# Optimization experiments

Measured on AMD Instinct MI355X. Metric: run time of the kernel, lower is better.

## Reference

```python
import jax, jax.numpy as jnp
import numpy as np

B, S, D, BS = 256, 256, 448, 32
NB = D // BS  # 14 diagonal blocks


def setup_inputs() -> dict:
    key = jax.random.key(0)
    ks = jax.random.split(key, 9)
    xavier = float(np.sqrt(6.0 / (D + D)))
    inp = {
        "x": jax.random.normal(ks[0], (B, S, D), jnp.float32),
        "W_q": jax.random.uniform(ks[1], (D, D), jnp.float32, -xavier, xavier),
        "W_k": jax.random.uniform(ks[2], (D, D), jnp.float32, -xavier, xavier),
        "W_v": jax.random.uniform(ks[3], (D, D), jnp.float32, -xavier, xavier),
        "W_o": jax.random.uniform(ks[4], (D, D), jnp.float32, -xavier, xavier),
        "SSM_A": jnp.tril(jax.random.normal(ks[5], (D, D), jnp.float32) * 0.001),
        "SSM_B": jnp.tril(jax.random.normal(ks[6], (D, D), jnp.float32) * 0.001),
        "SSM_C": jnp.tril(jax.random.normal(ks[7], (D, D), jnp.float32) * 0.001),
        "dynamic_weight": jnp.full((1,), 0.5, jnp.float32),  # torch init value
        "ln_gamma": jnp.ones((D,), jnp.float32),
        "ln_beta": jnp.zeros((D,), jnp.float32),
    }
    return inp


def _diag_blocks(M):
    # extract the NB diagonal 32x32 blocks: [NB, BS, BS]
    idx = jnp.arange(NB)
    return M.reshape(NB, BS, NB, BS)[idx, :, idx, :]


def _block_linear(x, M):
    # block-diagonal matmul, vectorized over all 14 blocks at once
    xr = x.reshape(B, S, NB, BS)
    return jnp.einsum('bsni,nij->bsnj', xr, _diag_blocks(M)).reshape(B, S, D)


def _block_quadratic(x, M):
    # einsum('bsi,ij,bsk->bsj') per block == (x_blk @ M_blk) * sum_k(x_blk) * 0.1
    xr = x.reshape(B, S, NB, BS)
    y = jnp.einsum('bsni,nij->bsnj', xr, _diag_blocks(M))
    y = y * (jnp.sum(xr, axis=-1, keepdims=True) * 0.1)
    return y.reshape(B, S, D)


def _layer_norm(x, gamma, beta):
    mu = jnp.mean(x, axis=-1, keepdims=True)
    var = jnp.mean(jnp.square(x - mu), axis=-1, keepdims=True)
    return (x - mu) * jax.lax.rsqrt(var + 1e-5) * gamma + beta


def reference(x, W_q, W_k, W_v, W_o, SSM_A, SSM_B, SSM_C, dynamic_weight, ln_gamma, ln_beta):
    q = jnp.einsum('bsi,id->bsd', x, W_q)
    k = jnp.einsum('bsi,id->bsd', x, W_k)
    v = jnp.einsum('bsi,id->bsd', x, W_v)
    dw = jax.nn.sigmoid(dynamic_weight)  # sigmoid(0.5)=0.622 -> blended branch (seq_len == threshold)
    ssm_lin = _layer_norm(
        _block_linear(q, SSM_A) + _block_linear(k, SSM_B) + _block_linear(v, SSM_C),
        ln_gamma, ln_beta)
    ssm_quad = _layer_norm(
        _block_quadratic(q, SSM_A) + _block_quadratic(k, SSM_B) + _block_quadratic(v, SSM_C),
        ln_gamma, ln_beta)
    ssm = dw * ssm_quad + (1.0 - dw) * ssm_lin
    ssm = ssm + x  # residual; dropout is identity in eval mode
    return jnp.einsum('bsd,do->bso', ssm, W_o)
```

## Files before the change

kernel.cpp:

```cpp
#include <hip/hip_runtime.h>
#include <hip/hip_bf16.h>


typedef unsigned short u16;
typedef unsigned int u32;
typedef __bf16 bf16x8 __attribute__((ext_vector_type(8)));
typedef float f32x4 __attribute__((ext_vector_type(4)));

#define D_DIM 448
#define M_DIM 65536
#define NCAT 1386
#define NCAT_PAD 1408
#define N2_PAD 512

__device__ __forceinline__ u16 f2bf(float f) {
    union { float f; u32 u; } v; v.f = f;
    u32 u = v.u;
    u32 r = (u + 0x7fffu + ((u >> 16) & 1u)) >> 16;
    return (u16)r;
}
__device__ __forceinline__ float bf2f(u16 h) {
    union { u32 u; float f; } v; v.u = ((u32)h) << 16;
    return v.f;
}

__device__ __forceinline__ void load_lds16(const void* g, void* l) {
    __builtin_amdgcn_global_load_lds(
        (const __attribute__((address_space(1))) void*)g,
        (__attribute__((address_space(3))) void*)l, 16, 0, 0);
}

__global__ __launch_bounds__(64) void prep_wcat(
    const float* __restrict__ Wq, const float* __restrict__ Wk, const float* __restrict__ Wv,
    const float* __restrict__ SA, const float* __restrict__ SB, const float* __restrict__ SC,
    u16* __restrict__ WcatT)
{
    const int j = blockIdx.x;
    const int lane = threadIdx.x;
    u16* dst = WcatT + (size_t)j * D_DIM;

    if (j >= NCAT) {
        for (int t = lane; t < D_DIM; t += 64) dst[t] = 0;
        return;
    }
    if (j < 3 * D_DIM) {
        const int g = j / D_DIM, jj = j % D_DIM, n = jj >> 5;
        const float* W = (g == 0) ? Wq : (g == 1) ? Wk : Wv;
        const float* Mm = (g == 0) ? SA : (g == 1) ? SB : SC;
        __shared__ float av[32];
        if (lane < 32) av[lane] = Mm[(size_t)(n * 32 + lane) * D_DIM + jj];
        __syncthreads();
        for (int t = lane; t < D_DIM; t += 64) {
            const float* wrow = W + (size_t)t * D_DIM + n * 32;
            float s = 0.f;
            #pragma unroll
            for (int l = 0; l < 32; ++l) s += wrow[l] * av[l];
            dst[t] = f2bf(s);
        }
    } else {
        const int js = j - 3 * D_DIM;
        const int g = js / 14, n = js % 14;
        const float* W = (g == 0) ? Wq : (g == 1) ? Wk : Wv;
        for (int t = lane; t < D_DIM; t += 64) {
            const float* wrow = W + (size_t)t * D_DIM + n * 32;
            float s = 0.f;
            #pragma unroll
            for (int l = 0; l < 32; ++l) s += wrow[l];
            dst[t] = f2bf(0.1f * s);
        }
    }
}

__global__ __launch_bounds__(256) void prep_wo(const float* __restrict__ Wo, u16* __restrict__ WoT) {
    const int idx = blockIdx.x * 256 + threadIdx.x;
    const int o = idx / D_DIM, d = idx % D_DIM;
    WoT[idx] = (o < D_DIM) ? f2bf(Wo[(size_t)d * D_DIM + o]) : (u16)0;
}

__global__ __launch_bounds__(256) void cvt_x_kernel(const float* __restrict__ x, u16* __restrict__ xb) {
    const size_t i = ((size_t)blockIdx.x * 256 + threadIdx.x) * 4;
    float4 v = *reinterpret_cast<const float4*>(x + i);
    u16 o0 = f2bf(v.x), o1 = f2bf(v.y), o2 = f2bf(v.z), o3 = f2bf(v.w);
    u32 lo = (u32)o0 | ((u32)o1 << 16);
    u32 hi = (u32)o2 | ((u32)o3 << 16);
    u32* p = reinterpret_cast<u32*>(xb + i);
    p[0] = lo; p[1] = hi;
}

template<bool BF16OUT>
__global__ __launch_bounds__(256) void gemm_bt(
    const u16* __restrict__ A,
    const u16* __restrict__ Bt,
    void* __restrict__ Cout,
    int ldc, int nreal, int ncolblk)
{
    __shared__ u16 lA[2][128 * 32];
    __shared__ u16 lB[2][128 * 32];
    const int tid = threadIdx.x;
    const int wave = tid >> 6, lane = tid & 63;

    const int cpx = gridDim.x >> 3;
    const int bid = blockIdx.x;
    const int t = (bid & 7) * cpx + (bid >> 3);
    const int bx = t % ncolblk, by = t / ncolblk;
    const int brow = by * 128, bcol = bx * 128;
    const int wr = wave >> 1, wc = wave & 1;

    f32x4 acc[4][4];
    #pragma unroll
    for (int i = 0; i < 4; ++i)
        #pragma unroll
        for (int j = 0; j < 4; ++j) {
            f32x4 z = {0.f, 0.f, 0.f, 0.f};
            acc[i][j] = z;
        }

    const int lrow = lane & 15;
    const int kgrp = (lane >> 4) << 3;

    for (int kt = 0; kt < 7; ++kt) {
        const int k0 = kt * 64;
        #pragma unroll
        for (int ks = 0; ks < 2; ++ks) {
            const int kb = k0 + ks * 32;
            #pragma unroll
            for (int i = 0; i < 2; ++i) {
                const int chunk = (wave * 2 + i) * 64 + lane;
                const int row = chunk >> 2, kk = (chunk & 3) << 3;
                load_lds16(A + (size_t)(brow + row) * D_DIM + kb + kk,
                           &lA[ks][(wave * 2 + i) * 512]);
                load_lds16(Bt + (size_t)(bcol + row) * D_DIM + kb + kk,
                           &lB[ks][(wave * 2 + i) * 512]);
            }
        }
        __syncthreads();

        #pragma unroll
        for (int ks = 0; ks < 2; ++ks) {
            bf16x8 af[4];
            #pragma unroll
            for (int mi = 0; mi < 4; ++mi) {
                const int r = wr * 64 + mi * 16 + lrow;
                af[mi] = *reinterpret_cast<const bf16x8*>(&lA[ks][r * 32 + kgrp]);
            }
            #pragma unroll
            for (int ni = 0; ni < 4; ++ni) {
                const int n = wc * 64 + ni * 16 + lrow;
                bf16x8 bfr = *reinterpret_cast<const bf16x8*>(&lB[ks][n * 32 + kgrp]);
                #pragma unroll
                for (int mi = 0; mi < 4; ++mi)
                    acc[mi][ni] = __builtin_amdgcn_mfma_f32_16x16x32_bf16(af[mi], bfr, acc[mi][ni], 0, 0, 0);
            }
        }
        __syncthreads();
    }

    const int rbase = brow + wr * 64 + ((lane >> 4) << 2);
    const int cbase = bcol + wc * 64 + (lane & 15);
    #pragma unroll
    for (int mi = 0; mi < 4; ++mi) {
        #pragma unroll
        for (int ni = 0; ni < 4; ++ni) {
            const int col = cbase + ni * 16;
            #pragma unroll
            for (int r = 0; r < 4; ++r) {
                const int row = rbase + mi * 16 + r;
                const float v = acc[mi][ni][r];
                if (BF16OUT) {
                    ((u16*)Cout)[(size_t)row * ldc + col] = f2bf(v);
                } else {
                    if (col < nreal)
                        ((float*)Cout)[(size_t)row * nreal + col] = v;
                }
            }
        }
    }
}

__global__ __launch_bounds__(256) void ssm_epilogue(
    const u16* __restrict__ Z, const u16* __restrict__ xb,
    const float* __restrict__ gamma, const float* __restrict__ beta,
    const float* __restrict__ dynw, u16* __restrict__ ssm)
{
    const int row = blockIdx.x * 4 + (threadIdx.x >> 6);
    const int lane = threadIdx.x & 63;
    const u16* zr = Z + (size_t)row * NCAT_PAD;
    const float dwv = 1.0f / (1.0f + __expf(-dynw[0]));
    const bool act = lane < 56;
    const int j0 = lane * 8;
    const int n = lane >> 2;

    float sv = (lane < 42) ? bf2f(zr[1344 + lane]) : 0.f;
    const float sA = __shfl(sv, n);
    const float sB = __shfl(sv, 14 + n);
    const float sC = __shfl(sv, 28 + n);

    float L[8], Q[8];
    float s0 = 0.f, s1 = 0.f, s2 = 0.f, s3 = 0.f;
    if (act) {
        uint4 va = *reinterpret_cast<const uint4*>(zr + j0);
        uint4 vb = *reinterpret_cast<const uint4*>(zr + 448 + j0);
        uint4 vc = *reinterpret_cast<const uint4*>(zr + 896 + j0);
        const u32* pa = reinterpret_cast<const u32*>(&va);
        const u32* pb = reinterpret_cast<const u32*>(&vb);
        const u32* pc = reinterpret_cast<const u32*>(&vc);
        #pragma unroll
        for (int w = 0; w < 4; ++w) {
            #pragma unroll
            for (int h = 0; h < 2; ++h) {
                const int i = w * 2 + h;
                const float a = bf2f((u16)((pa[w] >> (16 * h)) & 0xffffu));
                const float b = bf2f((u16)((pb[w] >> (16 * h)) & 0xffffu));
                const float c = bf2f((u16)((pc[w] >> (16 * h)) & 0xffffu));
                const float Lv = a + b + c;
                const float Qv = a * sA + b * sB + c * sC;
                L[i] = Lv; Q[i] = Qv;
                s0 += Lv; s1 += Lv * Lv; s2 += Qv; s3 += Qv * Qv;
            }
        }
    } else {
        #pragma unroll
        for (int i = 0; i < 8; ++i) { L[i] = 0.f; Q[i] = 0.f; }
    }
    #pragma unroll
    for (int off = 32; off > 0; off >>= 1) {
        s0 += __shfl_xor(s0, off);
        s1 += __shfl_xor(s1, off);
        s2 += __shfl_xor(s2, off);
        s3 += __shfl_xor(s3, off);
    }
    const float inv = 1.0f / 448.0f;
    const float mu0 = s0 * inv, mu1 = s2 * inv;
    const float rs0 = rsqrtf(fmaxf(s1 * inv - mu0 * mu0, 0.f) + 1e-5f);
    const float rs1 = rsqrtf(fmaxf(s3 * inv - mu1 * mu1, 0.f) + 1e-5f);

    if (act) {
        float4 g0 = *reinterpret_cast<const float4*>(gamma + j0);
        float4 g1 = *reinterpret_cast<const float4*>(gamma + j0 + 4);
        float4 b0 = *reinterpret_cast<const float4*>(beta + j0);
        float4 b1 = *reinterpret_cast<const float4*>(beta + j0 + 4);
        const float* gp = &g0.x;
        float gv[8] = {g0.x, g0.y, g0.z, g0.w, g1.x, g1.y, g1.z, g1.w};
        float bv[8] = {b0.x, b0.y, b0.z, b0.w, b1.x, b1.y, b1.z, b1.w};
        (void)gp;
        uint4 vx = *reinterpret_cast<const uint4*>(xb + (size_t)row * D_DIM + j0);
        const u32* px = reinterpret_cast<const u32*>(&vx);
        u32 outw[4];
        #pragma unroll
        for (int w = 0; w < 4; ++w) {
            u16 h0, h1;
            {
                const int i = w * 2;
                const float xr = bf2f((u16)(px[w] & 0xffffu));
                const float ln = (L[i] - mu0) * rs0 * gv[i] + bv[i];
                const float qn = (Q[i] - mu1) * rs1 * gv[i] + bv[i];
                h0 = f2bf(dwv * qn + (1.0f - dwv) * ln + xr);
            }
            {
                const int i = w * 2 + 1;
                const float xr = bf2f((u16)(px[w] >> 16));
                const float ln = (L[i] - mu0) * rs0 * gv[i] + bv[i];
                const float qn = (Q[i] - mu1) * rs1 * gv[i] + bv[i];
                h1 = f2bf(dwv * qn + (1.0f - dwv) * ln + xr);
            }
            outw[w] = (u32)h0 | ((u32)h1 << 16);
        }
        uint4 ov = {outw[0], outw[1], outw[2], outw[3]};
        *reinterpret_cast<uint4*>(ssm + (size_t)row * D_DIM + j0) = ov;
    }
}

extern "C" void kernel_launch(void* const* d_in, const int* in_sizes, int n_in,
                              void* d_out, int out_size, void* d_ws, size_t ws_size,
                              hipStream_t stream) {
    const float* x    = (const float*)d_in[0];
    const float* Wq   = (const float*)d_in[1];
    const float* Wk   = (const float*)d_in[2];
    const float* Wv   = (const float*)d_in[3];
    const float* Wo   = (const float*)d_in[4];
    const float* SA   = (const float*)d_in[5];
    const float* SB   = (const float*)d_in[6];
    const float* SC   = (const float*)d_in[7];
    const float* dynw = (const float*)d_in[8];
    const float* gma  = (const float*)d_in[9];
    const float* bta  = (const float*)d_in[10];
    float* out = (float*)d_out;

    char* ws = (char*)d_ws;
    u16* Xbf   = (u16*)(ws);
    u16* WcatT = (u16*)(ws + 58720256);
    u16* WoT   = (u16*)(ws + 59981824);
    u16* Z     = (u16*)(ws + 60440576);

    prep_wcat<<<dim3(NCAT_PAD), dim3(64), 0, stream>>>(Wq, Wk, Wv, SA, SB, SC, WcatT);
    prep_wo<<<dim3(896), dim3(256), 0, stream>>>(Wo, WoT);
    cvt_x_kernel<<<dim3(28672), dim3(256), 0, stream>>>(x, Xbf);

    gemm_bt<true><<<dim3(5632), dim3(256), 0, stream>>>(
        Xbf, WcatT, (void*)Z, NCAT_PAD, NCAT_PAD, 11);

    ssm_epilogue<<<dim3(M_DIM / 4), dim3(256), 0, stream>>>(Z, Xbf, gma, bta, dynw, Xbf);

    gemm_bt<false><<<dim3(2048), dim3(256), 0, stream>>>(
        Xbf, WoT, (void*)out, 448, 448, 4);
}
```

Measured before the change: 449.0 us.

## Merge prep kernels into one launch and double-buffer GEMM k-loop

Folds the three preprocessing kernels (x conversion, W_o transpose, Wcat build) into one kernel dispatched by block index, which saves two launches. The GEMM k-loop now uses ping-pong LDS buffers with 32-wide k stages, so global-to-LDS loads for the next stage are issued before the MFMAs on the current stage. This overlaps memory and compute, but the loop runs 14 stages instead of 7, which adds barriers. In the merged prep kernel the Wcat blocks now run 256 threads where only 64 were used before, so many threads sit idle.

```diff
diff --git a/kernel.cpp b/kernel.cpp
--- a/kernel.cpp
+++ b/kernel.cpp
@@ -13,6 +13,10 @@
 #define NCAT_PAD 1408
 #define N2_PAD 512
 
+#define CVT_BLKS 28672
+#define WO_BLKS 896
+#define WCAT_BLKS 1408
+
 __device__ __forceinline__ u16 f2bf(float f) {
     union { float f; u32 u; } v; v.f = f;
     u32 u = v.u;
@@ -30,17 +34,35 @@
         (__attribute__((address_space(3))) void*)l, 16, 0, 0);
 }
 
-__global__ __launch_bounds__(64) void prep_wcat(
+__global__ __launch_bounds__(256) void prep_all(
+    const float* __restrict__ x,
     const float* __restrict__ Wq, const float* __restrict__ Wk, const float* __restrict__ Wv,
+    const float* __restrict__ Wo,
     const float* __restrict__ SA, const float* __restrict__ SB, const float* __restrict__ SC,
-    u16* __restrict__ WcatT)
+    u16* __restrict__ Xbf, u16* __restrict__ WcatT, u16* __restrict__ WoT)
 {
-    const int j = blockIdx.x;
-    const int lane = threadIdx.x;
+    const int bid = blockIdx.x;
+    const int tid = threadIdx.x;
+
+    if (bid < CVT_BLKS) {
+        const size_t i = ((size_t)bid * 256 + tid) * 4;
+        float4 v = *reinterpret_cast<const float4*>(x + i);
+        u32 lo = (u32)f2bf(v.x) | ((u32)f2bf(v.y) << 16);
+        u32 hi = (u32)f2bf(v.z) | ((u32)f2bf(v.w) << 16);
+        u32* p = reinterpret_cast<u32*>(Xbf + i);
+        p[0] = lo; p[1] = hi;
+        return;
+    }
+    if (bid < CVT_BLKS + WO_BLKS) {
+        const int idx = (bid - CVT_BLKS) * 256 + tid;
+        const int o = idx / D_DIM, d = idx % D_DIM;
+        WoT[idx] = (o < D_DIM) ? f2bf(Wo[(size_t)d * D_DIM + o]) : (u16)0;
+        return;
+    }
+    const int j = bid - (CVT_BLKS + WO_BLKS);
     u16* dst = WcatT + (size_t)j * D_DIM;
-
     if (j >= NCAT) {
-        for (int t = lane; t < D_DIM; t += 64) dst[t] = 0;
+        for (int t = tid; t < D_DIM; t += 256) dst[t] = 0;
         return;
     }
     if (j < 3 * D_DIM) {
@@ -48,9 +70,9 @@
         const float* W = (g == 0) ? Wq : (g == 1) ? Wk : Wv;
         const float* Mm = (g == 0) ? SA : (g == 1) ? SB : SC;
         __shared__ float av[32];
-        if (lane < 32) av[lane] = Mm[(size_t)(n * 32 + lane) * D_DIM + jj];
+        if (tid < 32) av[tid] = Mm[(size_t)(n * 32 + tid) * D_DIM + jj];
         __syncthreads();
-        for (int t = lane; t < D_DIM; t += 64) {
+        for (int t = tid; t < D_DIM; t += 256) {
             const float* wrow = W + (size_t)t * D_DIM + n * 32;
             float s = 0.f;
             #pragma unroll
@@ -61,7 +83,7 @@
         const int js = j - 3 * D_DIM;
         const int g = js / 14, n = js % 14;
         const float* W = (g == 0) ? Wq : (g == 1) ? Wk : Wv;
-        for (int t = lane; t < D_DIM; t += 64) {
+        for (int t = tid; t < D_DIM; t += 256) {
             const float* wrow = W + (size_t)t * D_DIM + n * 32;
             float s = 0.f;
             #pragma unroll
@@ -69,22 +91,6 @@
             dst[t] = f2bf(0.1f * s);
         }
     }
-}
-
-__global__ __launch_bounds__(256) void prep_wo(const float* __restrict__ Wo, u16* __restrict__ WoT) {
-    const int idx = blockIdx.x * 256 + threadIdx.x;
-    const int o = idx / D_DIM, d = idx % D_DIM;
-    WoT[idx] = (o < D_DIM) ? f2bf(Wo[(size_t)d * D_DIM + o]) : (u16)0;
-}
-
-__global__ __launch_bounds__(256) void cvt_x_kernel(const float* __restrict__ x, u16* __restrict__ xb) {
-    const size_t i = ((size_t)blockIdx.x * 256 + threadIdx.x) * 4;
-    float4 v = *reinterpret_cast<const float4*>(x + i);
-    u16 o0 = f2bf(v.x), o1 = f2bf(v.y), o2 = f2bf(v.z), o3 = f2bf(v.w);
-    u32 lo = (u32)o0 | ((u32)o1 << 16);
-    u32 hi = (u32)o2 | ((u32)o3 << 16);
-    u32* p = reinterpret_cast<u32*>(xb + i);
-    p[0] = lo; p[1] = hi;
 }
 
 template<bool BF16OUT>
@@ -94,8 +100,7 @@
     void* __restrict__ Cout,
     int ldc, int nreal, int ncolblk)
 {
-    __shared__ u16 lA[2][128 * 32];
-    __shared__ u16 lB[2][128 * 32];
+    __shared__ u16 lA0[4096], lB0[4096], lA1[4096], lB1[4096];
     const int tid = threadIdx.x;
     const int wave = tid >> 6, lane = tid & 63;
 
@@ -110,50 +115,58 @@
     #pragma unroll
     for (int i = 0; i < 4; ++i)
         #pragma unroll
-        for (int j = 0; j < 4; ++j) {
+        for (int jj = 0; jj < 4; ++jj) {
             f32x4 z = {0.f, 0.f, 0.f, 0.f};
-            acc[i][j] = z;
+            acc[i][jj] = z;
         }
 
     const int lrow = lane & 15;
     const int kgrp = (lane >> 4) << 3;
 
-    for (int kt = 0; kt < 7; ++kt) {
-        const int k0 = kt * 64;
-        #pragma unroll
-        for (int ks = 0; ks < 2; ++ks) {
-            const int kb = k0 + ks * 32;
-            #pragma unroll
-            for (int i = 0; i < 2; ++i) {
-                const int chunk = (wave * 2 + i) * 64 + lane;
-                const int row = chunk >> 2, kk = (chunk & 3) << 3;
-                load_lds16(A + (size_t)(brow + row) * D_DIM + kb + kk,
-                           &lA[ks][(wave * 2 + i) * 512]);
-                load_lds16(Bt + (size_t)(bcol + row) * D_DIM + kb + kk,
-                           &lB[ks][(wave * 2 + i) * 512]);
-            }
-        }
+    const int c0 = wave * 128 + lane;
+    const int c1 = c0 + 64;
+    const int row0 = c0 >> 2, kk0 = (c0 & 3) << 3;
+    const int row1 = c1 >> 2, kk1 = (c1 & 3) << 3;
+    const u16* ga0 = A  + (size_t)(brow + row0) * D_DIM + kk0;
+    const u16* ga1 = A  + (size_t)(brow + row1) * D_DIM + kk1;
+    const u16* gb0 = Bt + (size_t)(bcol + row0) * D_DIM + kk0;
+    const u16* gb1 = Bt + (size_t)(bcol + row1) * D_DIM + kk1;
+    const int d0 = wave * 1024, d1 = wave * 1024 + 512;
+
+#define STAGE(LA, LB, koff) do { \
+    load_lds16(ga0 + (koff), &LA[d0]); \
+    load_lds16(ga1 + (koff), &LA[d1]); \
+    load_lds16(gb0 + (koff), &LB[d0]); \
+    load_lds16(gb1 + (koff), &LB[d1]); \
+} while (0)
+
+#define COMPUTE(LA, LB) do { \
+    bf16x8 af[4]; \
+    _Pragma("unroll") \
+    for (int mi = 0; mi < 4; ++mi) \
+        af[mi] = *reinterpret_cast<const bf16x8*>(&LA[(wr * 64 + mi * 16 + lrow) * 32 + kgrp]); \
+    _Pragma("unroll") \
+    for (int ni = 0; ni < 4; ++ni) { \
+        bf16x8 bfr = *reinterpret_cast<const bf16x8*>(&LB[(wc * 64 + ni * 16 + lrow) * 32 + kgrp]); \
+        _Pragma("unroll") \
+        for (int mi = 0; mi < 4; ++mi) \
+            acc[mi][ni] = __builtin_amdgcn_mfma_f32_16x16x32_bf16(af[mi], bfr, acc[mi][ni], 0, 0, 0); \
+    } \
+} while (0)
+
+    STAGE(lA0, lB0, 0);
+    __syncthreads();
+
+    for (int kt = 0; kt < 14; kt += 2) {
+        STAGE(lA1, lB1, (kt + 1) * 32);
+        COMPUTE(lA0, lB0);
         __syncthreads();
-
-        #pragma unroll
-        for (int ks = 0; ks < 2; ++ks) {
-            bf16x8 af[4];
-            #pragma unroll
-            for (int mi = 0; mi < 4; ++mi) {
-                const int r = wr * 64 + mi * 16 + lrow;
-                af[mi] = *reinterpret_cast<const bf16x8*>(&lA[ks][r * 32 + kgrp]);
-            }
-            #pragma unroll
-            for (int ni = 0; ni < 4; ++ni) {
-                const int n = wc * 64 + ni * 16 + lrow;
-                bf16x8 bfr = *reinterpret_cast<const bf16x8*>(&lB[ks][n * 32 + kgrp]);
-                #pragma unroll
-                for (int mi = 0; mi < 4; ++mi)
-                    acc[mi][ni] = __builtin_amdgcn_mfma_f32_16x16x32_bf16(af[mi], bfr, acc[mi][ni], 0, 0, 0);
-            }
-        }
+        if (kt + 2 < 14) STAGE(lA0, lB0, (kt + 2) * 32);
+        COMPUTE(lA1, lB1);
         __syncthreads();
     }
+#undef STAGE
+#undef COMPUTE
 
     const int rbase = brow + wr * 64 + ((lane >> 4) << 2);
     const int cbase = bcol + wc * 64 + (lane & 15);
@@ -239,10 +252,8 @@
         float4 g1 = *reinterpret_cast<const float4*>(gamma + j0 + 4);
         float4 b0 = *reinterpret_cast<const float4*>(beta + j0);
         float4 b1 = *reinterpret_cast<const float4*>(beta + j0 + 4);
-        const float* gp = &g0.x;
         float gv[8] = {g0.x, g0.y, g0.z, g0.w, g1.x, g1.y, g1.z, g1.w};
         float bv[8] = {b0.x, b0.y, b0.z, b0.w, b1.x, b1.y, b1.z, b1.w};
-        (void)gp;
         uint4 vx = *reinterpret_cast<const uint4*>(xb + (size_t)row * D_DIM + j0);
         const u32* px = reinterpret_cast<const u32*>(&vx);
         u32 outw[4];
@@ -292,9 +303,8 @@
     u16* WoT   = (u16*)(ws + 59981824);
     u16* Z     = (u16*)(ws + 60440576);
 
-    prep_wcat<<<dim3(NCAT_PAD), dim3(64), 0, stream>>>(Wq, Wk, Wv, SA, SB, SC, WcatT);
-    prep_wo<<<dim3(896), dim3(256), 0, stream>>>(Wo, WoT);
-    cvt_x_kernel<<<dim3(28672), dim3(256), 0, stream>>>(x, Xbf);
+    prep_all<<<dim3(CVT_BLKS + WO_BLKS + WCAT_BLKS), dim3(256), 0, stream>>>(
+        x, Wq, Wk, Wv, Wo, SA, SB, SC, Xbf, WcatT, WoT);
 
     gemm_bt<true><<<dim3(5632), dim3(256), 0, stream>>>(
         Xbf, WcatT, (void*)Z, NCAT_PAD, NCAT_PAD, 11);
```

Result: faster. 432.4 us (-3.7%).
